# Kernel optimization log

Measured on AMD Instinct MI355X. Metric: run time of the kernel, lower is better.

Reference implementation:

```python
import jax, jax.numpy as jnp
import numpy as np
from jax import lax

S, LC = 4096, 16          # words per sentence, chars per word (padded/fixed)
CHARSET, VOCAB, TAGS = 128, 100000, 50
CDIM, WDIM, H, F = 10, 250, 250, 32


def setup_inputs() -> dict:
    key = jax.random.key(0)
    ks = jax.random.split(key, 12)
    s = 0.05
    return {
        "char_indices": jax.random.randint(ks[0], (S, LC), 0, CHARSET),
        "word_indices": jax.random.randint(ks[1], (S,), 0, VOCAB),
        "char_emb": jax.random.normal(ks[2], (CHARSET, CDIM), jnp.float32) * s,
        "word_emb": jax.random.normal(ks[3], (VOCAB, WDIM), jnp.float32) * s,
        "conv_w": jax.random.normal(ks[4], (F, CDIM, 3), jnp.float32) * s,
        "conv_b": jax.random.normal(ks[5], (F,), jnp.float32) * s,
        "W_ih": jax.random.normal(ks[6], (4 * H, WDIM + F), jnp.float32) * s,
        "W_hh": jax.random.normal(ks[7], (4 * H, H), jnp.float32) * s,
        "b_ih": jax.random.normal(ks[8], (4 * H,), jnp.float32) * s,
        "b_hh": jax.random.normal(ks[9], (4 * H,), jnp.float32) * s,
        "dense_w": jax.random.normal(ks[10], (TAGS, H), jnp.float32) * s,
        "dense_b": jax.random.normal(ks[11], (TAGS,), jnp.float32) * s,
    }


def _forward(char_indices, word_indices, char_emb, word_emb, conv_w, conv_b,
             W_ih, W_hh, b_ih, b_hh, dense_w, dense_b):
    # Char CNN, batched over all S words at once (original loops per word).
    ce = char_emb[char_indices]                 # [S, LC, CDIM]
    ce = jnp.transpose(ce, (0, 2, 1))           # [S, CDIM, LC]  (NCH)
    conv = lax.conv_general_dilated(
        ce, conv_w, window_strides=(1,), padding=[(1, 1)],
        dimension_numbers=("NCH", "OIH", "NCH"))  # [S, F, LC]
    conv = conv + conv_b[None, :, None]
    char_feat = jnp.max(conv, axis=2)           # [S, F] (max over time)

    x = jnp.concatenate([char_feat, word_emb[word_indices]], axis=1)  # [S, F+WDIM]

    # Single-layer LSTM, batch=1, PyTorch gate order i,f,g,o.
    xg = x @ W_ih.T + (b_ih + b_hh)             # [S, 4H] precompute input part

    def step(carry, xg_t):
        h, c = carry
        gates = xg_t + W_hh @ h                 # [4H]
        i, f, g, o = jnp.split(gates, 4)
        i, f, o = jax.nn.sigmoid(i), jax.nn.sigmoid(f), jax.nn.sigmoid(o)
        g = jnp.tanh(g)
        c = f * c + i * g
        h = o * jnp.tanh(c)
        return (h, c), h

    h0 = jnp.zeros((H,), x.dtype)
    c0 = jnp.zeros((H,), x.dtype)
    _, hs = lax.scan(step, (h0, c0), xg)        # [S, H]

    logits = hs @ dense_w.T + dense_b           # [S, TAGS]
    return jax.nn.log_softmax(logits, axis=1)


def reference(char_indices, word_indices, char_emb, word_emb, conv_w, conv_b,
              W_ih, W_hh, b_ih, b_hh, dense_w, dense_b):
    return _forward(char_indices, word_indices, char_emb, word_emb, conv_w,
                    conv_b, W_ih, W_hh, b_ih, b_hh, dense_w, dense_b)
```

## Files before the change

kernel.cpp:

```cpp
#include <hip/hip_runtime.h>
#include <hip/hip_bf16.h>
#include <hip/hip_fp16.h>


typedef _Float16 h2 __attribute__((ext_vector_type(2)));

__device__ __forceinline__ float dot2(unsigned int w, unsigned int h, float acc) {
#if __has_builtin(__builtin_amdgcn_fdot2)
    return __builtin_amdgcn_fdot2(__builtin_bit_cast(h2, w),
                                  __builtin_bit_cast(h2, h), acc, false);
#else
    h2 a = __builtin_bit_cast(h2, w), b = __builtin_bit_cast(h2, h);
    return acc + (float)a[0] * (float)b[0] + (float)a[1] * (float)b[1];
#endif
}

__global__ void prep_kernel(const float* __restrict__ whh,
                            uint4* __restrict__ wpackE) {
    int id = blockIdx.x * 256 + threadIdx.x;
    if (id >= 32768) return;
    int tid = id & 511;
    int rest = id >> 9;
    int u = rest & 3, J = (rest >> 2) & 7, m = rest >> 5;
    int row = 2 * tid + m;
    unsigned ww[4];
#pragma unroll
    for (int c = 0; c < 4; ++c) {
        int p = J * 16 + u * 4 + c;
        float e0 = (row < 1000 && 2 * p < 250) ? whh[row * 250 + 2 * p] : 0.0f;
        float e1 = (row < 1000 && 2 * p + 1 < 250) ? whh[row * 250 + 2 * p + 1] : 0.0f;
        h2 hp; hp[0] = (_Float16)e0; hp[1] = (_Float16)e1;
        ww[c] = __builtin_bit_cast(unsigned, hp);
    }
    uint4 v; v.x = ww[0]; v.y = ww[1]; v.z = ww[2]; v.w = ww[3];
    wpackE[rest * 512 + tid] = v;
}

__global__ __launch_bounds__(256) void build_xt(
    const int* __restrict__ ci, const int* __restrict__ wi,
    const float* __restrict__ cemb, const float* __restrict__ wemb,
    const float* __restrict__ convw, const float* __restrict__ convb,
    float* __restrict__ xT) {
    __shared__ float ce[64][16][10];
    __shared__ float cw[32][30];
    __shared__ float cb[32];
    __shared__ int widx[64];
    const int tid = threadIdx.x;
    const int w0 = blockIdx.x * 64;

    for (int i = tid; i < 960; i += 256) cw[i / 30][i % 30] = convw[i];
    if (tid < 32) cb[tid] = convb[tid];
    if (tid < 64) widx[tid] = wi[w0 + tid];
    for (int i = tid; i < 1024; i += 256) {
        int w = i >> 4, lc = i & 15;
        int idx = ci[(w0 + w) * 16 + lc];
#pragma unroll
        for (int c = 0; c < 10; ++c) ce[w][lc][c] = cemb[idx * 10 + c];
    }
    __syncthreads();

    for (int i = tid; i < 2048; i += 256) {
        int w = i >> 5, f = i & 31;
        float mx = -1e30f;
        for (int t = 0; t < 16; ++t) {
            float s = cb[f];
#pragma unroll
            for (int dt = 0; dt < 3; ++dt) {
                int tt = t + dt - 1;
                if (tt >= 0 && tt < 16) {
#pragma unroll
                    for (int c = 0; c < 10; ++c)
                        s += ce[w][tt][c] * cw[f][c * 3 + dt];
                }
            }
            mx = fmaxf(mx, s);
        }
        xT[f * 4096 + w0 + w] = mx;
    }
    for (int i = tid; i < 64 * 250; i += 256) {
        int w = i & 63, jj = i >> 6;
        xT[(32 + jj) * 4096 + w0 + w] = wemb[(long)widx[w] * 250 + jj];
    }
}

__global__ __launch_bounds__(256) void xg_gemm(
    const float* __restrict__ wih,
    const float* __restrict__ xT,
    const float* __restrict__ bih, const float* __restrict__ bhh,
    float* __restrict__ xg) {
    const int g = blockIdx.y * 256 + threadIdx.x;
    const int gg = (g < 1000) ? g : 999;
    const int w0 = blockIdx.x * 16;
    float acc[16];
#pragma unroll
    for (int i = 0; i < 16; ++i) acc[i] = 0.0f;
    const float* wrow = wih + gg * 282;
    for (int k = 0; k < 282; ++k) {
        float wv = wrow[k];
        const float* xrow = xT + k * 4096 + w0;
#pragma unroll
        for (int i = 0; i < 16; ++i) acc[i] = fmaf(wv, xrow[i], acc[i]);
    }
    if (g < 1000) {
        float b = bih[g] + bhh[g];
#pragma unroll
        for (int i = 0; i < 16; ++i) xg[(w0 + i) * 1000 + g] = acc[i] + b;
    }
}

__global__ __launch_bounds__(512, 2) void lstm_scan(
    const uint4* __restrict__ wpackE,
    const float* __restrict__ xg,
    float* __restrict__ hsf32) {
    __shared__ unsigned lds_h[128];
    __shared__ float lds_gates[1000];

    const int tid = threadIdx.x;
    const bool act_on = (tid < 500);
    const int row0 = act_on ? 2 * tid : 996;
    const bool isg = (tid >= 250) & (tid < 375);

    uint4 wq[2][8][4];
#pragma unroll
    for (int m = 0; m < 2; ++m)
#pragma unroll
        for (int J = 0; J < 8; ++J)
#pragma unroll
            for (int u = 0; u < 4; ++u)
                wq[m][J][u] = wpackE[((m * 8 + J) * 4 + u) * 512 + tid];

    if (tid < 128) lds_h[tid] = 0u;
    float cc0 = 0.0f, cc1 = 0.0f;
    __syncthreads();

    float2 xg_cur = *(const float2*)&xg[row0];

#pragma unroll 1
    for (int t = 0; t < 4096; ++t) {
        const int tn = (t + 1 < 4096) ? t + 1 : 4095;
        float2 xg_nxt = *(const float2*)&xg[tn * 1000 + row0];

        float a0 = xg_cur.x, a1 = xg_cur.y;
#pragma unroll
        for (int J = 0; J < 8; ++J) {
            uint4 h0 = *(const uint4*)&lds_h[J * 16];
            uint4 h1 = *(const uint4*)&lds_h[J * 16 + 4];
            uint4 hx2 = *(const uint4*)&lds_h[J * 16 + 8];
            uint4 h3 = *(const uint4*)&lds_h[J * 16 + 12];
            a0 = dot2(wq[0][J][0].x, h0.x, a0); a0 = dot2(wq[0][J][0].y, h0.y, a0);
            a0 = dot2(wq[0][J][0].z, h0.z, a0); a0 = dot2(wq[0][J][0].w, h0.w, a0);
            a0 = dot2(wq[0][J][1].x, h1.x, a0); a0 = dot2(wq[0][J][1].y, h1.y, a0);
            a0 = dot2(wq[0][J][1].z, h1.z, a0); a0 = dot2(wq[0][J][1].w, h1.w, a0);
            a0 = dot2(wq[0][J][2].x, hx2.x, a0); a0 = dot2(wq[0][J][2].y, hx2.y, a0);
            a0 = dot2(wq[0][J][2].z, hx2.z, a0); a0 = dot2(wq[0][J][2].w, hx2.w, a0);
            a0 = dot2(wq[0][J][3].x, h3.x, a0); a0 = dot2(wq[0][J][3].y, h3.y, a0);
            a0 = dot2(wq[0][J][3].z, h3.z, a0); a0 = dot2(wq[0][J][3].w, h3.w, a0);
            a1 = dot2(wq[1][J][0].x, h0.x, a1); a1 = dot2(wq[1][J][0].y, h0.y, a1);
            a1 = dot2(wq[1][J][0].z, h0.z, a1); a1 = dot2(wq[1][J][0].w, h0.w, a1);
            a1 = dot2(wq[1][J][1].x, h1.x, a1); a1 = dot2(wq[1][J][1].y, h1.y, a1);
            a1 = dot2(wq[1][J][1].z, h1.z, a1); a1 = dot2(wq[1][J][1].w, h1.w, a1);
            a1 = dot2(wq[1][J][2].x, hx2.x, a1); a1 = dot2(wq[1][J][2].y, hx2.y, a1);
            a1 = dot2(wq[1][J][2].z, hx2.z, a1); a1 = dot2(wq[1][J][2].w, hx2.w, a1);
            a1 = dot2(wq[1][J][3].x, h3.x, a1); a1 = dot2(wq[1][J][3].y, h3.y, a1);
            a1 = dot2(wq[1][J][3].z, h3.z, a1); a1 = dot2(wq[1][J][3].w, h3.w, a1);
        }

        {
            float e0 = __expf(isg ? 2.0f * a0 : -a0);
            float e1 = __expf(isg ? 2.0f * a1 : -a1);
            float s0 = __builtin_amdgcn_rcpf(1.0f + e0);
            float s1 = __builtin_amdgcn_rcpf(1.0f + e1);
            float v0 = isg ? fmaf(-2.0f, s0, 1.0f) : s0;
            float v1 = isg ? fmaf(-2.0f, s1, 1.0f) : s1;
            if (act_on) *(float2*)&lds_gates[2 * tid] = make_float2(v0, v1);
        }
        __syncthreads();

        if (tid < 125) {
            float2 gi = *(const float2*)&lds_gates[2 * tid];
            float2 gf = *(const float2*)&lds_gates[250 + 2 * tid];
            float2 gg = *(const float2*)&lds_gates[500 + 2 * tid];
            float2 go = *(const float2*)&lds_gates[750 + 2 * tid];
            cc0 = fmaf(gf.x, cc0, gi.x * gg.x);
            cc1 = fmaf(gf.y, cc1, gi.y * gg.y);
            float e0 = __expf(2.0f * cc0), e1 = __expf(2.0f * cc1);
            float t0 = fmaf(-2.0f, __builtin_amdgcn_rcpf(1.0f + e0), 1.0f);
            float t1 = fmaf(-2.0f, __builtin_amdgcn_rcpf(1.0f + e1), 1.0f);
            float h0 = go.x * t0;
            float h1 = go.y * t1;
            *(float2*)&hsf32[t * 250 + 2 * tid] = make_float2(h0, h1);
            h2 hp; hp[0] = (_Float16)h0; hp[1] = (_Float16)h1;
            lds_h[tid] = __builtin_bit_cast(unsigned, hp);
        }
        __syncthreads();
        xg_cur = xg_nxt;
    }
}

__global__ __launch_bounds__(256) void dense_lsm(
    const float* __restrict__ hs, const float* __restrict__ dw,
    const float* __restrict__ db, float* __restrict__ out) {
    const int wave = threadIdx.x >> 6, lane = threadIdx.x & 63;
    const int s = blockIdx.x * 4 + wave;
    const int tag = lane;
    float acc = -1e30f;
    if (tag < 50) {
        acc = db[tag];
        const float* h = hs + (long)s * 250;
        const float* wrow = dw + tag * 250;
        for (int k = 0; k < 250; ++k) acc = fmaf(h[k], wrow[k], acc);
    }
    float m = acc;
#pragma unroll
    for (int off = 32; off; off >>= 1) m = fmaxf(m, __shfl_xor(m, off));
    float e = (tag < 50) ? expf(acc - m) : 0.0f;
    float ssum = e;
#pragma unroll
    for (int off = 32; off; off >>= 1) ssum += __shfl_xor(ssum, off);
    if (tag < 50) out[(long)s * 50 + tag] = acc - m - logf(ssum);
}

extern "C" void kernel_launch(void* const* d_in, const int* in_sizes, int n_in,
                              void* d_out, int out_size, void* d_ws, size_t ws_size,
                              hipStream_t stream) {
    const int*   ci    = (const int*)d_in[0];
    const int*   wi    = (const int*)d_in[1];
    const float* cemb  = (const float*)d_in[2];
    const float* wemb  = (const float*)d_in[3];
    const float* convw = (const float*)d_in[4];
    const float* convb = (const float*)d_in[5];
    const float* wih   = (const float*)d_in[6];
    const float* whh   = (const float*)d_in[7];
    const float* bih   = (const float*)d_in[8];
    const float* bhh   = (const float*)d_in[9];
    const float* dw    = (const float*)d_in[10];
    const float* db    = (const float*)d_in[11];
    float* out = (float*)d_out;

    char* ws = (char*)d_ws;
    constexpr size_t OFF_WPE = 0;
    constexpr size_t OFF_XG  = 524288;
    constexpr size_t OFF_HSF = 16908288;
    constexpr size_t OFF_XT  = OFF_HSF;

    uint4* wpackE = (uint4*)(ws + OFF_WPE);
    float* xg     = (float*)(ws + OFF_XG);
    float* hsf32  = (float*)(ws + OFF_HSF);
    float* xT     = (float*)(ws + OFF_XT);

    prep_kernel<<<dim3(128), dim3(256), 0, stream>>>(whh, wpackE);
    build_xt<<<dim3(64), dim3(256), 0, stream>>>(ci, wi, cemb, wemb, convw,
                                                 convb, xT);
    xg_gemm<<<dim3(256, 4), dim3(256), 0, stream>>>(wih, xT, bih, bhh, xg);
    lstm_scan<<<dim3(1), dim3(512), 0, stream>>>(wpackE, xg, hsf32);
    dense_lsm<<<dim3(1024), dim3(256), 0, stream>>>(hsf32, dw, db, out);
}
```

Before: 11.92 ms.

## Split recurrent weights between registers and LDS in LSTM scan

Repacks W_hh so 3/4 of each thread's fp16 weight slice stays in VGPRs and the last quarter (columns 192-255) moves to LDS, read each timestep. Previously all 128 uint4 lived in registers, which likely caused spilling or register pressure at 512 threads. An asm barrier pins the register portion, and waves_per_eu is set explicitly. In exchange, every step now does extra LDS reads for the weight tail, and lds_wt takes 128KB of shared memory.

```diff
diff --git a/kernel.cpp b/kernel.cpp
--- a/kernel.cpp
+++ b/kernel.cpp
@@ -16,24 +16,27 @@
 }
 
 __global__ void prep_kernel(const float* __restrict__ whh,
-                            uint4* __restrict__ wpackE) {
+                            uint4* __restrict__ wpackF) {
     int id = blockIdx.x * 256 + threadIdx.x;
     if (id >= 32768) return;
     int tid = id & 511;
-    int rest = id >> 9;
-    int u = rest & 3, J = (rest >> 2) & 7, m = rest >> 5;
+    int gu = id >> 9;
+    int m, p0;
+    if (gu < 48) { m = gu / 24; int u = gu % 24; p0 = 4 * u; }
+    else         { int gt = gu - 48; m = gt >> 3; p0 = 96 + 4 * (gt & 7); }
     int row = 2 * tid + m;
+    if (row > 999) row = 998 + m;
     unsigned ww[4];
 #pragma unroll
     for (int c = 0; c < 4; ++c) {
-        int p = J * 16 + u * 4 + c;
-        float e0 = (row < 1000 && 2 * p < 250) ? whh[row * 250 + 2 * p] : 0.0f;
-        float e1 = (row < 1000 && 2 * p + 1 < 250) ? whh[row * 250 + 2 * p + 1] : 0.0f;
+        int p = p0 + c;
+        float e0 = (2 * p < 250)     ? whh[row * 250 + 2 * p]     : 0.0f;
+        float e1 = (2 * p + 1 < 250) ? whh[row * 250 + 2 * p + 1] : 0.0f;
         h2 hp; hp[0] = (_Float16)e0; hp[1] = (_Float16)e1;
         ww[c] = __builtin_bit_cast(unsigned, hp);
     }
     uint4 v; v.x = ww[0]; v.y = ww[1]; v.z = ww[2]; v.w = ww[3];
-    wpackE[rest * 512 + tid] = v;
+    wpackF[(gu << 9) + tid] = v;
 }
 
 __global__ __launch_bounds__(256) void build_xt(
@@ -108,10 +111,17 @@
     }
 }
 
-__global__ __launch_bounds__(512, 2) void lstm_scan(
-    const uint4* __restrict__ wpackE,
+#define DOT4(ACC, W, H)                                                     \
+    ACC = dot2((W).x, (H).x, ACC); ACC = dot2((W).y, (H).y, ACC);           \
+    ACC = dot2((W).z, (H).z, ACC); ACC = dot2((W).w, (H).w, ACC);
+
+__global__ __launch_bounds__(512)
+__attribute__((amdgpu_waves_per_eu(2, 2)))
+void lstm_scan(
+    const uint4* __restrict__ wpackF,
     const float* __restrict__ xg,
     float* __restrict__ hsf32) {
+    __shared__ uint4 lds_wt[16 * 512];
     __shared__ unsigned lds_h[128];
     __shared__ float lds_gates[1000];
 
@@ -120,14 +130,22 @@
     const int row0 = act_on ? 2 * tid : 996;
     const bool isg = (tid >= 250) & (tid < 375);
 
-    uint4 wq[2][8][4];
+    uint4 wq[2][24];
 #pragma unroll
     for (int m = 0; m < 2; ++m)
 #pragma unroll
-        for (int J = 0; J < 8; ++J)
-#pragma unroll
-            for (int u = 0; u < 4; ++u)
-                wq[m][J][u] = wpackE[((m * 8 + J) * 4 + u) * 512 + tid];
+        for (int u = 0; u < 24; ++u)
+            wq[m][u] = wpackF[((m * 24 + u) << 9) + tid];
+#pragma unroll
+    for (int m = 0; m < 2; ++m)
+#pragma unroll
+        for (int u = 0; u < 24; ++u)
+            asm volatile("" : "+v"(wq[m][u].x), "+v"(wq[m][u].y),
+                              "+v"(wq[m][u].z), "+v"(wq[m][u].w));
+
+#pragma unroll
+    for (int g = 0; g < 16; ++g)
+        lds_wt[(g << 9) + tid] = wpackF[((48 + g) << 9) + tid];
 
     if (tid < 128) lds_h[tid] = 0u;
     float cc0 = 0.0f, cc1 = 0.0f;
@@ -141,28 +159,25 @@
         float2 xg_nxt = *(const float2*)&xg[tn * 1000 + row0];
 
         float a0 = xg_cur.x, a1 = xg_cur.y;
-#pragma unroll
-        for (int J = 0; J < 8; ++J) {
+
+#pragma unroll
+        for (int J = 0; J < 6; ++J) {
             uint4 h0 = *(const uint4*)&lds_h[J * 16];
             uint4 h1 = *(const uint4*)&lds_h[J * 16 + 4];
-            uint4 hx2 = *(const uint4*)&lds_h[J * 16 + 8];
+            uint4 hx = *(const uint4*)&lds_h[J * 16 + 8];
             uint4 h3 = *(const uint4*)&lds_h[J * 16 + 12];
-            a0 = dot2(wq[0][J][0].x, h0.x, a0); a0 = dot2(wq[0][J][0].y, h0.y, a0);
-            a0 = dot2(wq[0][J][0].z, h0.z, a0); a0 = dot2(wq[0][J][0].w, h0.w, a0);
-            a0 = dot2(wq[0][J][1].x, h1.x, a0); a0 = dot2(wq[0][J][1].y, h1.y, a0);
-            a0 = dot2(wq[0][J][1].z, h1.z, a0); a0 = dot2(wq[0][J][1].w, h1.w, a0);
-            a0 = dot2(wq[0][J][2].x, hx2.x, a0); a0 = dot2(wq[0][J][2].y, hx2.y, a0);
-            a0 = dot2(wq[0][J][2].z, hx2.z, a0); a0 = dot2(wq[0][J][2].w, hx2.w, a0);
-            a0 = dot2(wq[0][J][3].x, h3.x, a0); a0 = dot2(wq[0][J][3].y, h3.y, a0);
-            a0 = dot2(wq[0][J][3].z, h3.z, a0); a0 = dot2(wq[0][J][3].w, h3.w, a0);
-            a1 = dot2(wq[1][J][0].x, h0.x, a1); a1 = dot2(wq[1][J][0].y, h0.y, a1);
-            a1 = dot2(wq[1][J][0].z, h0.z, a1); a1 = dot2(wq[1][J][0].w, h0.w, a1);
-            a1 = dot2(wq[1][J][1].x, h1.x, a1); a1 = dot2(wq[1][J][1].y, h1.y, a1);
-            a1 = dot2(wq[1][J][1].z, h1.z, a1); a1 = dot2(wq[1][J][1].w, h1.w, a1);
-            a1 = dot2(wq[1][J][2].x, hx2.x, a1); a1 = dot2(wq[1][J][2].y, hx2.y, a1);
-            a1 = dot2(wq[1][J][2].z, hx2.z, a1); a1 = dot2(wq[1][J][2].w, hx2.w, a1);
-            a1 = dot2(wq[1][J][3].x, h3.x, a1); a1 = dot2(wq[1][J][3].y, h3.y, a1);
-            a1 = dot2(wq[1][J][3].z, h3.z, a1); a1 = dot2(wq[1][J][3].w, h3.w, a1);
+            DOT4(a0, wq[0][4 * J + 0], h0) DOT4(a0, wq[0][4 * J + 1], h1)
+            DOT4(a0, wq[0][4 * J + 2], hx) DOT4(a0, wq[0][4 * J + 3], h3)
+            DOT4(a1, wq[1][4 * J + 0], h0) DOT4(a1, wq[1][4 * J + 1], h1)
+            DOT4(a1, wq[1][4 * J + 2], hx) DOT4(a1, wq[1][4 * J + 3], h3)
+        }
+#pragma unroll
+        for (int c = 0; c < 8; ++c) {
+            uint4 hh = *(const uint4*)&lds_h[96 + 4 * c];
+            uint4 t0 = lds_wt[(c << 9) + tid];
+            uint4 t1 = lds_wt[((8 + c) << 9) + tid];
+            DOT4(a0, t0, hh)
+            DOT4(a1, t1, hh)
         }
 
         {
@@ -238,20 +253,20 @@
     float* out = (float*)d_out;
 
     char* ws = (char*)d_ws;
-    constexpr size_t OFF_WPE = 0;
+    constexpr size_t OFF_WPF = 0;
     constexpr size_t OFF_XG  = 524288;
     constexpr size_t OFF_HSF = 16908288;
     constexpr size_t OFF_XT  = OFF_HSF;
 
-    uint4* wpackE = (uint4*)(ws + OFF_WPE);
+    uint4* wpackF = (uint4*)(ws + OFF_WPF);
     float* xg     = (float*)(ws + OFF_XG);
     float* hsf32  = (float*)(ws + OFF_HSF);
     float* xT     = (float*)(ws + OFF_XT);
 
-    prep_kernel<<<dim3(128), dim3(256), 0, stream>>>(whh, wpackE);
+    prep_kernel<<<dim3(128), dim3(256), 0, stream>>>(whh, wpackF);
     build_xt<<<dim3(64), dim3(256), 0, stream>>>(ci, wi, cemb, wemb, convw,
                                                  convb, xT);
     xg_gemm<<<dim3(256, 4), dim3(256), 0, stream>>>(wih, xT, bih, bhh, xg);
-    lstm_scan<<<dim3(1), dim3(512), 0, stream>>>(wpackE, xg, hsf32);
+    lstm_scan<<<dim3(1), dim3(512), 0, stream>>>(wpackF, xg, hsf32);
     dense_lsm<<<dim3(1024), dim3(256), 0, stream>>>(hsf32, dw, db, out);
 }
```

After: 30.53 ms. +156.2%, slower.
